# Performance work log

Measured on AMD Instinct MI355X. Metric: run time of the kernel, lower is better.

Reference implementation:

```python
import jax, jax.numpy as jnp
import numpy as np

D_IN = 64      # num_in_features
D_OUT = 64     # num_out_features
H = 512        # neurons_per_layer
M = 64         # num_meta_in_features
META_OUT = D_IN * H + H + H * D_OUT + D_OUT  # 66112
B = 2048


def setup_inputs() -> dict:
    key = jax.random.key(0)
    k1, k2, k3 = jax.random.split(key, 3)
    x = jax.random.normal(k1, (B, D_IN + M), dtype=jnp.float32)
    # xavier-normal-ish init for the two hypernet linears, zero biases
    W_in = jax.random.normal(k2, (H, M), dtype=jnp.float32) * jnp.sqrt(2.0 / (H + M))
    b_in = jnp.zeros((H,), dtype=jnp.float32)
    W_out = jax.random.normal(k3, (META_OUT, H), dtype=jnp.float32) * jnp.sqrt(2.0 / (META_OUT + H))
    b_out = jnp.zeros((META_OUT,), dtype=jnp.float32)
    return {"x": x, "W_in": W_in, "b_in": b_in, "W_out": W_out, "b_out": b_out}


def reference(x, W_in, b_in, W_out, b_out):
    real = x[:, :D_IN]            # [B, D_IN]
    meta = x[:, D_IN:]            # [B, M]
    h = jax.nn.elu(meta @ W_in.T + b_in)          # [B, H]
    gen = h @ W_out.T + b_out                     # [B, META_OUT]
    base = D_IN * H
    l_in_w = gen[:, :base].reshape(-1, D_IN, H)   # [B, D_IN, H]
    l_in_b = gen[:, base:base + H]                # [B, H]
    base += H
    add = H * D_OUT
    l_out_w = gen[:, base:base + add].reshape(-1, H, D_OUT)  # [B, H, D_OUT]
    l_out_b = gen[:, base + add:]                 # [B, D_OUT]
    # tensordot(real, l_in_w, dims=([1],[1])).diagonal(0,1).T == per-sample matvec
    y = jax.nn.elu(jnp.einsum('bi,bih->bh', real, l_in_w) + l_in_b)
    out = jnp.einsum('bh,bho->bo', y, l_out_w) + l_out_b
    return out
```

## Files before the change

kernel.cpp:

```cpp
#include <hip/hip_runtime.h>
#include <hip/hip_bf16.h>
#include <stdint.h>

#define B_N   2048
#define XW    128
#define KDIM  512
#define NROWS_W   66112
#define NROWS_PAD 66560

typedef __bf16 v8bf  __attribute__((ext_vector_type(8)));
typedef float  f32x4 __attribute__((ext_vector_type(4)));

__device__ __forceinline__ unsigned short f2bf(float f) {
    uint32_t u = __float_as_uint(f);
    u += 0x7FFF + ((u >> 16) & 1);
    return (unsigned short)(u >> 16);
}
__device__ __forceinline__ float bf2f(unsigned short h) {
    return __uint_as_float(((uint32_t)h) << 16);
}
__device__ __forceinline__ float elu1(float v) {
    return v > 0.0f ? v : expm1f(v);
}
__device__ __forceinline__ void gload_lds16(const void* g, void* l) {
    __builtin_amdgcn_global_load_lds(
        (const __attribute__((address_space(1))) unsigned int*)g,
        (__attribute__((address_space(3))) unsigned int*)l, 16, 0, 0);
}

__global__ void k_h(const float* __restrict__ x, const float* __restrict__ W_in,
                    const float* __restrict__ b_in, unsigned short* __restrict__ hb) {
    int idx = blockIdx.x * 256 + threadIdx.x;
    int b = idx >> 9, j = idx & 511;
    const float4* xm = (const float4*)(x + (size_t)b * XW + 64);
    const float4* wr = (const float4*)(W_in + (size_t)j * 64);
    float acc = 0.f;
#pragma unroll
    for (int q = 0; q < 16; ++q) {
        float4 a = xm[q], w = wr[q];
        acc += a.x * w.x + a.y * w.y + a.z * w.z + a.w * w.w;
    }
    acc = elu1(acc + b_in[j]);
    hb[idx] = f2bf(acc);
}

__global__ void k_conv(const float* __restrict__ Wf, unsigned short* __restrict__ Wb) {
    size_t c = (size_t)blockIdx.x * 256 + threadIdx.x;
    size_t row = c >> 6; int kk = (int)(c & 63);
    union { uint4 v; unsigned short u[8]; } o;
    o.v = (uint4){0, 0, 0, 0};
    if (row < NROWS_W) {
        const float* wp = Wf + row * KDIM + kk * 8;
        float4 w0 = *(const float4*)wp, w1 = *(const float4*)(wp + 4);
        o.u[0] = f2bf(w0.x); o.u[1] = f2bf(w0.y); o.u[2] = f2bf(w0.z); o.u[3] = f2bf(w0.w);
        o.u[4] = f2bf(w1.x); o.u[5] = f2bf(w1.y); o.u[6] = f2bf(w1.z); o.u[7] = f2bf(w1.w);
    }
    *(uint4*)(Wb + c * 8) = o.v;
}

template<int MODE, bool BF16B>
__global__ __launch_bounds__(512, 2)
void k_pgemm(const unsigned short* __restrict__ hb,
             const unsigned short* __restrict__ Wb,
             const float* __restrict__ Wf,
             const float* __restrict__ scaleSrc,
             float* __restrict__ outAcc) {
    constexpr int NP   = MODE ? 129 : 130;
    constexpr int OUTW = MODE ? 64 : 512;
    constexpr int SCW  = MODE ? 36 : 9;
    constexpr int NSPLIT = 16;

    __shared__ char smem[131072 + 128 * SCW * 4];
    char* As = smem;
    char* Bs = smem + 65536;
    float* sc = (float*)(smem + 131072);

    const int tid = threadIdx.x;
    const int m0  = blockIdx.x * 128;
    const int s   = blockIdx.y;
    const int pBeg = (NP * s) / NSPLIT;
    const int pEnd = (NP * (s + 1)) / NSPLIT;
    const int halfS = (MODE == 0 && pBeg >= 65) ? 1 : 0;
    const int iBeg  = pBeg - halfS * 65;

    const int wid = tid >> 6, l = tid & 63;
    const int lr = l & 15, lg = l >> 4;
    const int wm = wid >> 2, wn = wid & 3;

    for (int c = tid; c < 128 * SCW; c += 512) {
        int row = c / SCW, j = c - row * SCW;
        float v = 1.0f;
        if (MODE == 0) {
            int i = iBeg + j;
            if (i < 64) v = scaleSrc[(size_t)(m0 + row) * XW + i];
        } else {
            int g = pBeg * 4 + j;
            if (g < 512) v = scaleSrc[(size_t)(m0 + row) * KDIM + g];
        }
        sc[c] = v;
    }

    int aB[4], aX[4], bB[4], bX[4];
#pragma unroll
    for (int q = 0; q < 4; ++q) {
        int ra = wm * 64 + q * 16 + lr;
        aB[q] = ra * 512; aX[q] = (ra & 7) << 4;
        int rb = wn * 64 + q * 16 + lr;
        bB[q] = rb * 128; bX[q] = (rb & 7) << 4;
    }
    const int lgx = lg * 16;

    f32x4 accP[4][4], accO[4][4];
#pragma unroll
    for (int mi = 0; mi < 4; ++mi)
#pragma unroll
        for (int ni = 0; ni < 4; ++ni) {
            accP[mi][ni] = (f32x4){0.f, 0.f, 0.f, 0.f};
            accO[mi][ni] = (f32x4){0.f, 0.f, 0.f, 0.f};
        }

    for (int kh = 0; kh < 2; ++kh) {
#pragma unroll
        for (int q = 0; q < 8; ++q) {
            int c = q * 512 + tid;
            int row = c >> 5, kk = c & 31;
            uint4 v = *(const uint4*)(hb + (size_t)(m0 + row) * KDIM + kh * 256 + kk * 8);
            *(uint4*)(As + row * 512 + ((kk * 16) ^ ((row & 7) << 4))) = v;
        }
        auto stageB = [&](int buf, int p, int k0) {
            char* Bbuf = Bs + buf * 32768;
            int wrowBase = (MODE == 0) ? ((p - halfS * 65) * 512 + halfS * 256)
                                       : (33280 + p * 256);
            if (BF16B) {
                int kByte = kh * 512 + k0 * 128;
#pragma unroll
                for (int j = 0; j < 4; ++j) {
                    int rg = wid * 4 + j;
                    int rowLoc = rg * 8 + (l >> 3);
                    size_t src = (size_t)(wrowBase + rowLoc) * 1024 + kByte
                               + (((l & 7) * 16) ^ ((l >> 3) << 4));
                    gload_lds16((const char*)Wb + src, Bbuf + rg * 1024);
                }
            } else {
                int kf = kh * 256 + k0 * 64;
#pragma unroll
                for (int q = 0; q < 4; ++q) {
                    int c = q * 512 + tid;
                    int rowLoc = c >> 3, kk = c & 7;
                    int wrow = wrowBase + rowLoc;
                    union { uint4 v; unsigned short u[8]; } o;
                    o.v = (uint4){0, 0, 0, 0};
                    if (wrow < NROWS_W) {
                        const float* wp = Wf + (size_t)wrow * KDIM + kf + kk * 8;
                        float4 w0 = *(const float4*)wp, w1 = *(const float4*)(wp + 4);
                        o.u[0] = f2bf(w0.x); o.u[1] = f2bf(w0.y);
                        o.u[2] = f2bf(w0.z); o.u[3] = f2bf(w0.w);
                        o.u[4] = f2bf(w1.x); o.u[5] = f2bf(w1.y);
                        o.u[6] = f2bf(w1.z); o.u[7] = f2bf(w1.w);
                    }
                    *(uint4*)(Bbuf + rowLoc * 128 + ((kk * 16) ^ ((rowLoc & 7) << 4))) = o.v;
                }
            }
        };

        stageB(0, pBeg, 0);
        __syncthreads();
        int cur = 0;
        for (int p = pBeg; p < pEnd; ++p) {
#pragma unroll
            for (int k0 = 0; k0 < 4; ++k0) {
                bool isLast = (p == pEnd - 1) && (k0 == 3);
                if (!isLast) stageB(cur ^ 1, (k0 == 3) ? p + 1 : p, (k0 + 1) & 3);
                char* Bbuf = Bs + cur * 32768;
#pragma unroll
                for (int ks = 0; ks < 2; ++ks) {
                    v8bf af[4], bf[4];
                    int kk = (ks * 64 + lgx);
#pragma unroll
                    for (int mi = 0; mi < 4; ++mi)
                        af[mi] = *(const v8bf*)(As + aB[mi] + k0 * 128 + (kk ^ aX[mi]));
#pragma unroll
                    for (int ni = 0; ni < 4; ++ni)
                        bf[ni] = *(const v8bf*)(Bbuf + bB[ni] + (kk ^ bX[ni]));
#pragma unroll
                    for (int mi = 0; mi < 4; ++mi)
#pragma unroll
                        for (int ni = 0; ni < 4; ++ni)
                            accP[mi][ni] = __builtin_amdgcn_mfma_f32_16x16x32_bf16(
                                af[mi], bf[ni], accP[mi][ni], 0, 0, 0);
                }
                if (k0 == 3) {
                    int jj = MODE ? ((p - pBeg) * 4 + wn) : (p - pBeg);
#pragma unroll
                    for (int mi = 0; mi < 4; ++mi) {
                        int rb = wm * 64 + mi * 16 + lg * 4;
#pragma unroll
                        for (int r = 0; r < 4; ++r) {
                            float sv = sc[(rb + r) * SCW + jj];
#pragma unroll
                            for (int ni = 0; ni < 4; ++ni)
                                accO[mi][ni][r] += sv * accP[mi][ni][r];
                        }
#pragma unroll
                        for (int ni = 0; ni < 4; ++ni)
                            accP[mi][ni] = (f32x4){0.f, 0.f, 0.f, 0.f};
                    }
                }
                __syncthreads();
                cur ^= 1;
            }
        }
    }
#pragma unroll
    for (int mi = 0; mi < 4; ++mi)
#pragma unroll
        for (int ni = 0; ni < 4; ++ni)
#pragma unroll
            for (int r = 0; r < 4; ++r) {
                int row = wm * 64 + mi * 16 + lg * 4 + r;
                int col = MODE ? (ni * 16 + lr) : (halfS * 256 + wn * 64 + ni * 16 + lr);
                atomicAdd(outAcc + (size_t)(m0 + row) * OUTW + col, accO[mi][ni][r]);
            }
}

__global__ void k_fin_y(const float* __restrict__ ypre, const float* __restrict__ x,
                        const float* __restrict__ b_out, float* __restrict__ y) {
    int idx = blockIdx.x * 256 + threadIdx.x;
    int b = idx >> 9, hh = idx & 511;
    float acc = ypre[idx] + b_out[32768 + hh];
    const float* xr = x + (size_t)b * XW;
#pragma unroll 8
    for (int i = 0; i < 64; ++i)
        acc += xr[i] * b_out[i * 512 + hh];
    y[idx] = elu1(acc);
}

__global__ void k_fin_out(const float* __restrict__ y, const float* __restrict__ b_out,
                          float* __restrict__ out) {
    int idx = blockIdx.x * 256 + threadIdx.x;
    int b = idx >> 6, o = idx & 63;
    float acc = out[idx] + b_out[66048 + o];
    const float* yr = y + (size_t)b * 512;
#pragma unroll 8
    for (int hh = 0; hh < 512; ++hh)
        acc += yr[hh] * b_out[33280 + hh * 64 + o];
    out[idx] = acc;
}

extern "C" void kernel_launch(void* const* d_in, const int* in_sizes, int n_in,
                              void* d_out, int out_size, void* d_ws, size_t ws_size,
                              hipStream_t stream) {
    const float* x     = (const float*)d_in[0];
    const float* W_in  = (const float*)d_in[1];
    const float* b_in  = (const float*)d_in[2];
    const float* W_out = (const float*)d_in[3];
    const float* b_out = (const float*)d_in[4];
    float* out = (float*)d_out;

    char* ws = (char*)d_ws;
    unsigned short* hb = (unsigned short*)ws;
    float* ypre        = (float*)(ws + (2u << 20));
    float* yv          = (float*)(ws + (6u << 20));
    unsigned short* Wb = (unsigned short*)(ws + (10u << 20));
    const size_t NEED = (10u << 20) + (size_t)NROWS_PAD * KDIM * 2;
    const bool bf16b = ws_size >= NEED;

    hipMemsetAsync(ypre, 0, (size_t)B_N * 512 * 4, stream);
    hipMemsetAsync(out,  0, (size_t)B_N * 64 * 4, stream);

    k_h<<<(B_N * 512) / 256, 256, 0, stream>>>(x, W_in, b_in, hb);

    if (bf16b) {
        k_conv<<<(NROWS_PAD * KDIM / 8) / 256, 256, 0, stream>>>(W_out, Wb);
        k_pgemm<0, true><<<dim3(16, 16), 512, 0, stream>>>(hb, Wb, W_out, x, ypre);
        k_fin_y<<<(B_N * 512) / 256, 256, 0, stream>>>(ypre, x, b_out, yv);
        k_pgemm<1, true><<<dim3(16, 16), 512, 0, stream>>>(hb, Wb, W_out, yv, out);
    } else {
        k_pgemm<0, false><<<dim3(16, 16), 512, 0, stream>>>(hb, Wb, W_out, x, ypre);
        k_fin_y<<<(B_N * 512) / 256, 256, 0, stream>>>(ypre, x, b_out, yv);
        k_pgemm<1, false><<<dim3(16, 16), 512, 0, stream>>>(hb, Wb, W_out, yv, out);
    }
    k_fin_out<<<(B_N * 64) / 256, 256, 0, stream>>>(yv, b_out, out);
}
```

Baseline: 310.2 us.

## Retile fused hypernet GEMM to 128x128 tiles with 256 threads and finer pipelining

Splits each weight-chunk tile across a new grid dimension so every block computes 128x128 with 4 waves instead of 128x256 with 8 waves, halving LDS use so more blocks can be resident. K is staged in quarters with 64-wide B chunks, and explicit vmcnt waits plus raw s_barrier let the next chunk's global-to-LDS copy overlap compute. It also raises wave priority around the MFMA block, vectorizes the scale application through a transposed scale layout, and removes the fp32 weight fallback path. The hb A-tile is now reloaded per K quarter and twice as many blocks issue atomics, which adds traffic.

```diff
diff --git a/kernel.cpp b/kernel.cpp
--- a/kernel.cpp
+++ b/kernel.cpp
@@ -15,9 +15,6 @@
     uint32_t u = __float_as_uint(f);
     u += 0x7FFF + ((u >> 16) & 1);
     return (unsigned short)(u >> 16);
-}
-__device__ __forceinline__ float bf2f(unsigned short h) {
-    return __uint_as_float(((uint32_t)h) << 16);
 }
 __device__ __forceinline__ float elu1(float v) {
     return v > 0.0f ? v : expm1f(v);
@@ -58,43 +55,42 @@
     *(uint4*)(Wb + c * 8) = o.v;
 }
 
-template<int MODE, bool BF16B>
-__global__ __launch_bounds__(512, 2)
+template<int MODE>
+__global__ __launch_bounds__(256, 2)
 void k_pgemm(const unsigned short* __restrict__ hb,
              const unsigned short* __restrict__ Wb,
-             const float* __restrict__ Wf,
              const float* __restrict__ scaleSrc,
              float* __restrict__ outAcc) {
     constexpr int NP   = MODE ? 129 : 130;
     constexpr int OUTW = MODE ? 64 : 512;
-    constexpr int SCW  = MODE ? 36 : 9;
-    constexpr int NSPLIT = 16;
-
-    __shared__ char smem[131072 + 128 * SCW * 4];
+    constexpr int SCW  = MODE ? 18 : 9;
+
+    __shared__ char smem[65536 + SCW * 128 * 4];
     char* As = smem;
-    char* Bs = smem + 65536;
-    float* sc = (float*)(smem + 131072);
+    char* Bs = smem + 32768;
+    float* sc = (float*)(smem + 65536);
 
     const int tid = threadIdx.x;
     const int m0  = blockIdx.x * 128;
-    const int s   = blockIdx.y;
-    const int pBeg = (NP * s) / NSPLIT;
-    const int pEnd = (NP * (s + 1)) / NSPLIT;
+    const int nh  = blockIdx.y;
+    const int s   = blockIdx.z;
+    const int pBeg = (NP * s) >> 4;
+    const int pEnd = (NP * (s + 1)) >> 4;
     const int halfS = (MODE == 0 && pBeg >= 65) ? 1 : 0;
     const int iBeg  = pBeg - halfS * 65;
 
     const int wid = tid >> 6, l = tid & 63;
     const int lr = l & 15, lg = l >> 4;
-    const int wm = wid >> 2, wn = wid & 3;
-
-    for (int c = tid; c < 128 * SCW; c += 512) {
-        int row = c / SCW, j = c - row * SCW;
+    const int wm = wid >> 1, wn = wid & 1;
+
+    for (int c = tid; c < SCW * 128; c += 256) {
+        int jj = c >> 7, row = c & 127;
         float v = 1.0f;
         if (MODE == 0) {
-            int i = iBeg + j;
+            int i = iBeg + jj;
             if (i < 64) v = scaleSrc[(size_t)(m0 + row) * XW + i];
         } else {
-            int g = pBeg * 4 + j;
+            int g = (pBeg + (jj >> 1)) * 4 + nh * 2 + (jj & 1);
             if (g < 512) v = scaleSrc[(size_t)(m0 + row) * KDIM + g];
         }
         sc[c] = v;
@@ -104,11 +100,10 @@
 #pragma unroll
     for (int q = 0; q < 4; ++q) {
         int ra = wm * 64 + q * 16 + lr;
-        aB[q] = ra * 512; aX[q] = (ra & 7) << 4;
+        aB[q] = ra * 256; aX[q] = ra & 7;
         int rb = wn * 64 + q * 16 + lr;
-        bB[q] = rb * 128; bX[q] = (rb & 7) << 4;
-    }
-    const int lgx = lg * 16;
+        bB[q] = rb * 128; bX[q] = rb & 7;
+    }
 
     f32x4 accP[4][4], accO[4][4];
 #pragma unroll
@@ -119,94 +114,77 @@
             accO[mi][ni] = (f32x4){0.f, 0.f, 0.f, 0.f};
         }
 
-    for (int kh = 0; kh < 2; ++kh) {
+    for (int kq = 0; kq < 4; ++kq) {
 #pragma unroll
         for (int q = 0; q < 8; ++q) {
-            int c = q * 512 + tid;
-            int row = c >> 5, kk = c & 31;
-            uint4 v = *(const uint4*)(hb + (size_t)(m0 + row) * KDIM + kh * 256 + kk * 8);
-            *(uint4*)(As + row * 512 + ((kk * 16) ^ ((row & 7) << 4))) = v;
-        }
-        auto stageB = [&](int buf, int p, int k0) {
-            char* Bbuf = Bs + buf * 32768;
-            int wrowBase = (MODE == 0) ? ((p - halfS * 65) * 512 + halfS * 256)
-                                       : (33280 + p * 256);
-            if (BF16B) {
-                int kByte = kh * 512 + k0 * 128;
-#pragma unroll
-                for (int j = 0; j < 4; ++j) {
-                    int rg = wid * 4 + j;
-                    int rowLoc = rg * 8 + (l >> 3);
-                    size_t src = (size_t)(wrowBase + rowLoc) * 1024 + kByte
-                               + (((l & 7) * 16) ^ ((l >> 3) << 4));
-                    gload_lds16((const char*)Wb + src, Bbuf + rg * 1024);
-                }
-            } else {
-                int kf = kh * 256 + k0 * 64;
-#pragma unroll
-                for (int q = 0; q < 4; ++q) {
-                    int c = q * 512 + tid;
-                    int rowLoc = c >> 3, kk = c & 7;
-                    int wrow = wrowBase + rowLoc;
-                    union { uint4 v; unsigned short u[8]; } o;
-                    o.v = (uint4){0, 0, 0, 0};
-                    if (wrow < NROWS_W) {
-                        const float* wp = Wf + (size_t)wrow * KDIM + kf + kk * 8;
-                        float4 w0 = *(const float4*)wp, w1 = *(const float4*)(wp + 4);
-                        o.u[0] = f2bf(w0.x); o.u[1] = f2bf(w0.y);
-                        o.u[2] = f2bf(w0.z); o.u[3] = f2bf(w0.w);
-                        o.u[4] = f2bf(w1.x); o.u[5] = f2bf(w1.y);
-                        o.u[6] = f2bf(w1.z); o.u[7] = f2bf(w1.w);
-                    }
-                    *(uint4*)(Bbuf + rowLoc * 128 + ((kk * 16) ^ ((rowLoc & 7) << 4))) = o.v;
-                }
-            }
+            int c = q * 256 + tid;
+            int row = c >> 4, kk = c & 15;
+            uint4 v = *(const uint4*)(hb + (size_t)(m0 + row) * KDIM + kq * 128 + kk * 8);
+            *(uint4*)(As + row * 256 + ((kk ^ (row & 7)) << 4)) = v;
+        }
+        auto stageB = [&](int buf, int p, int k0c) {
+            int wrow = MODE ? (33280 + p * 256 + nh * 128)
+                            : ((p - halfS * 65) * 512 + halfS * 256 + nh * 128);
+            const int rsub = tid >> 3;
+            const int sl = (tid & 7) ^ (rsub & 7);
+            const unsigned short* src0 = Wb + (size_t)(wrow + rsub) * KDIM
+                                       + kq * 128 + k0c * 64 + sl * 8;
+            char* dst0 = Bs + buf * 16384 + tid * 16;
+#pragma unroll
+            for (int q = 0; q < 4; ++q)
+                gload_lds16(src0 + (size_t)q * 32 * KDIM, dst0 + q * 4096);
         };
-
         stageB(0, pBeg, 0);
         __syncthreads();
         int cur = 0;
         for (int p = pBeg; p < pEnd; ++p) {
 #pragma unroll
-            for (int k0 = 0; k0 < 4; ++k0) {
-                bool isLast = (p == pEnd - 1) && (k0 == 3);
-                if (!isLast) stageB(cur ^ 1, (k0 == 3) ? p + 1 : p, (k0 + 1) & 3);
-                char* Bbuf = Bs + cur * 32768;
+            for (int k0 = 0; k0 < 2; ++k0) {
+                const bool last = (p == pEnd - 1) && (k0 == 1);
+                if (!last) {
+                    stageB(cur ^ 1, k0 ? p + 1 : p, k0 ^ 1);
+                    asm volatile("s_waitcnt vmcnt(4)" ::: "memory");
+                } else {
+                    asm volatile("s_waitcnt vmcnt(0)" ::: "memory");
+                }
+                __builtin_amdgcn_s_barrier();
+                asm volatile("" ::: "memory");
+                char* Bbuf = Bs + cur * 16384;
+                __builtin_amdgcn_s_setprio(1);
 #pragma unroll
                 for (int ks = 0; ks < 2; ++ks) {
-                    v8bf af[4], bf[4];
-                    int kk = (ks * 64 + lgx);
+                    v8bf af[4], bfr[4];
+                    const int sA = k0 * 8 + ks * 4 + lg;
+                    const int sB = ks * 4 + lg;
 #pragma unroll
                     for (int mi = 0; mi < 4; ++mi)
-                        af[mi] = *(const v8bf*)(As + aB[mi] + k0 * 128 + (kk ^ aX[mi]));
+                        af[mi] = *(const v8bf*)(As + aB[mi] + ((sA ^ aX[mi]) << 4));
 #pragma unroll
                     for (int ni = 0; ni < 4; ++ni)
-                        bf[ni] = *(const v8bf*)(Bbuf + bB[ni] + (kk ^ bX[ni]));
+                        bfr[ni] = *(const v8bf*)(Bbuf + bB[ni] + ((sB ^ bX[ni]) << 4));
 #pragma unroll
                     for (int mi = 0; mi < 4; ++mi)
 #pragma unroll
                         for (int ni = 0; ni < 4; ++ni)
                             accP[mi][ni] = __builtin_amdgcn_mfma_f32_16x16x32_bf16(
-                                af[mi], bf[ni], accP[mi][ni], 0, 0, 0);
+                                af[mi], bfr[ni], accP[mi][ni], 0, 0, 0);
                 }
-                if (k0 == 3) {
-                    int jj = MODE ? ((p - pBeg) * 4 + wn) : (p - pBeg);
+                __builtin_amdgcn_s_setprio(0);
+                if (k0 == 1) {
+                    int jj = MODE ? ((p - pBeg) * 2 + wn) : (p - pBeg);
+                    const f32x4* scv = (const f32x4*)(sc + jj * 128);
 #pragma unroll
                     for (int mi = 0; mi < 4; ++mi) {
-                        int rb = wm * 64 + mi * 16 + lg * 4;
-#pragma unroll
-                        for (int r = 0; r < 4; ++r) {
-                            float sv = sc[(rb + r) * SCW + jj];
-#pragma unroll
-                            for (int ni = 0; ni < 4; ++ni)
-                                accO[mi][ni][r] += sv * accP[mi][ni][r];
+                        f32x4 sv = scv[wm * 16 + mi * 4 + lg];
+#pragma unroll
+                        for (int ni = 0; ni < 4; ++ni) {
+                            accO[mi][ni] += sv * accP[mi][ni];
+                            accP[mi][ni] = (f32x4){0.f, 0.f, 0.f, 0.f};
                         }
-#pragma unroll
-                        for (int ni = 0; ni < 4; ++ni)
-                            accP[mi][ni] = (f32x4){0.f, 0.f, 0.f, 0.f};
                     }
                 }
-                __syncthreads();
+                asm volatile("" ::: "memory");
+                __builtin_amdgcn_s_barrier();
                 cur ^= 1;
             }
         }
@@ -218,7 +196,8 @@
 #pragma unroll
             for (int r = 0; r < 4; ++r) {
                 int row = wm * 64 + mi * 16 + lg * 4 + r;
-                int col = MODE ? (ni * 16 + lr) : (halfS * 256 + wn * 64 + ni * 16 + lr);
+                int col = MODE ? (ni * 16 + lr)
+                               : (halfS * 256 + nh * 128 + wn * 64 + ni * 16 + lr);
                 atomicAdd(outAcc + (size_t)(m0 + row) * OUTW + col, accO[mi][ni][r]);
             }
 }
@@ -262,23 +241,18 @@
     float* ypre        = (float*)(ws + (2u << 20));
     float* yv          = (float*)(ws + (6u << 20));
     unsigned short* Wb = (unsigned short*)(ws + (10u << 20));
-    const size_t NEED = (10u << 20) + (size_t)NROWS_PAD * KDIM * 2;
-    const bool bf16b = ws_size >= NEED;
 
     hipMemsetAsync(ypre, 0, (size_t)B_N * 512 * 4, stream);
     hipMemsetAsync(out,  0, (size_t)B_N * 64 * 4, stream);
 
     k_h<<<(B_N * 512) / 256, 256, 0, stream>>>(x, W_in, b_in, hb);
-
-    if (bf16b) {
-        k_conv<<<(NROWS_PAD * KDIM / 8) / 256, 256, 0, stream>>>(W_out, Wb);
-        k_pgemm<0, true><<<dim3(16, 16), 512, 0, stream>>>(hb, Wb, W_out, x, ypre);
-        k_fin_y<<<(B_N * 512) / 256, 256, 0, stream>>>(ypre, x, b_out, yv);
-        k_pgemm<1, true><<<dim3(16, 16), 512, 0, stream>>>(hb, Wb, W_out, yv, out);
-    } else {
-        k_pgemm<0, false><<<dim3(16, 16), 512, 0, stream>>>(hb, Wb, W_out, x, ypre);
-        k_fin_y<<<(B_N * 512) / 256, 256, 0, stream>>>(ypre, x, b_out, yv);
-        k_pgemm<1, false><<<dim3(16, 16), 512, 0, stream>>>(hb, Wb, W_out, yv, out);
-    }
+    k_conv<<<(NROWS_PAD * KDIM / 8) / 256, 256, 0, stream>>>(W_out, Wb);
+
+    k_pgemm<0><<<dim3(16, 2, 16), 256, 0, stream>>>(hb, Wb, x, ypre);
+
+    k_fin_y<<<(B_N * 512) / 256, 256, 0, stream>>>(ypre, x, b_out, yv);
+
+    k_pgemm<1><<<dim3(16, 2, 16), 256, 0, stream>>>(hb, Wb, yv, out);
+
     k_fin_out<<<(B_N * 64) / 256, 256, 0, stream>>>(yv, b_out, out);
 }
```

Result: faster. 284.4 us (-8.3%).
